# Performance work log

Hardware: AMD Instinct MI355X
Metric: run time of the kernel (lower is better)

The kernel has to match this reference:

```python
import jax, jax.numpy as jnp
import numpy as np

N, E, D, H, Z = 100000, 1600000, 128, 256, 64


def _gconv(x, src, dst, W, b, n):
    # DGL GraphConv, norm='both': D_in^{-1/2} A D_out^{-1/2} x W + b
    ones = jnp.ones(src.shape, x.dtype)
    deg_out = jnp.clip(jax.ops.segment_sum(ones, src, num_segments=n), 1.0)
    deg_in = jnp.clip(jax.ops.segment_sum(ones, dst, num_segments=n), 1.0)
    h = x * (deg_out ** -0.5)[:, None]          # scale by src out-degree
    agg = jax.ops.segment_sum(h[src], dst, num_segments=n)  # SpMM gather/scatter
    return (agg * (deg_in ** -0.5)[:, None]) @ W + b


def setup_inputs() -> dict:
    key = jax.random.key(0)
    ks = jax.random.split(key, 8)
    return {
        "features": jax.random.normal(ks[0], (N, D), jnp.float32),
        "src": jax.random.randint(ks[1], (E,), 0, N, jnp.int32),
        "dst": jax.random.randint(ks[2], (E,), 0, N, jnp.int32),
        "eps": jax.random.normal(ks[3], (N, Z), jnp.float32),
        "W1": jax.random.normal(ks[4], (D, H), jnp.float32) * (1.0 / np.sqrt(D)),
        "b1": jnp.zeros((H,), jnp.float32),
        "W2": jax.random.normal(ks[5], (H, 2 * Z), jnp.float32) * (1.0 / np.sqrt(H)),
        "b2": jnp.zeros((2 * Z,), jnp.float32),
        "W3": jax.random.normal(ks[6], (Z, D), jnp.float32) * (1.0 / np.sqrt(Z)),
        "b3": jnp.zeros((D,), jnp.float32),
    }


def reference(features, src, dst, eps, W1, b1, W2, b2, W3, b3):
    n = features.shape[0]
    h = jax.nn.relu(_gconv(features, src, dst, W1, b1, n))
    mean_logvar = _gconv(h, src, dst, W2, b2, n)
    mean, log_var = jnp.split(mean_logvar, 2, axis=1)
    z = eps * jnp.exp(0.5 * log_var) + mean  # reparameterization
    recon = _gconv(z, src, dst, W3, b3, n)
    return recon, mean, log_var
```

## Files before the change

kernel.cpp:

```cpp
#include <hip/hip_runtime.h>
#include <math.h>


#define MAXD 64

typedef short short8 __attribute__((ext_vector_type(8)));
typedef float f32x4 __attribute__((ext_vector_type(4)));

__device__ __forceinline__ unsigned short f2bf(float f) {
  union { float f; unsigned u; } c; c.f = f;
  unsigned r = c.u + 0x7FFF + ((c.u >> 16) & 1);
  return (unsigned short)(r >> 16);
}
__device__ __forceinline__ float bf2f(unsigned short b) {
  return __builtin_bit_cast(float, (unsigned)b << 16);
}

__global__ __launch_bounds__(256) void k_hist4(const int* __restrict__ src,
    const int* __restrict__ dst, int* __restrict__ degout, int* __restrict__ cnt,
    int* __restrict__ ebuf, int E) {
  int t = blockIdx.x * 256 + threadIdx.x;
  int e0 = t * 4;
  if (e0 + 4 <= E) {
    int4 s4 = *(const int4*)(src + e0);
    int4 d4 = *(const int4*)(dst + e0);
    atomicAdd(&degout[s4.x], 1);
    atomicAdd(&degout[s4.y], 1);
    atomicAdd(&degout[s4.z], 1);
    atomicAdd(&degout[s4.w], 1);
    int p0 = atomicAdd(&cnt[d4.x], 1);
    int p1 = atomicAdd(&cnt[d4.y], 1);
    int p2 = atomicAdd(&cnt[d4.z], 1);
    int p3 = atomicAdd(&cnt[d4.w], 1);
    if (p0 < MAXD) __builtin_nontemporal_store(s4.x, &ebuf[d4.x * MAXD + p0]);
    if (p1 < MAXD) __builtin_nontemporal_store(s4.y, &ebuf[d4.y * MAXD + p1]);
    if (p2 < MAXD) __builtin_nontemporal_store(s4.z, &ebuf[d4.z * MAXD + p2]);
    if (p3 < MAXD) __builtin_nontemporal_store(s4.w, &ebuf[d4.w * MAXD + p3]);
  } else {
    for (int e = e0; e < E; e++) {
      int s = src[e], d = dst[e];
      atomicAdd(&degout[s], 1);
      int p = atomicAdd(&cnt[d], 1);
      if (p < MAXD) __builtin_nontemporal_store(s, &ebuf[d * MAXD + p]);
    }
  }
}

__global__ __launch_bounds__(256) void k_scale(const int* __restrict__ degout,
    const int* __restrict__ cnt, float* __restrict__ sout,
    float* __restrict__ sin_, int N) {
  int i = blockIdx.x * 256 + threadIdx.x;
  if (i >= N) return;
  int dO = degout[i]; if (dO < 1) dO = 1;
  int dI = cnt[i];    if (dI < 1) dI = 1;
  sout[i] = rsqrtf((float)dO);
  sin_[i] = rsqrtf((float)dI);
}

__global__ __launch_bounds__(256) void k_cvt(const float* __restrict__ in,
    unsigned short* __restrict__ out, int n) {
  int i = (blockIdx.x * 256 + threadIdx.x) * 4;
  if (i >= n) return;
  float4 f = *(const float4*)(in + i);
  unsigned lo = (unsigned)f2bf(f.x) | ((unsigned)f2bf(f.y) << 16);
  unsigned hi = (unsigned)f2bf(f.z) | ((unsigned)f2bf(f.w) << 16);
  uint2 o; o.x = lo; o.y = hi;
  *(uint2*)(out + i) = o;
}

template <int K, int OC>
__global__ __launch_bounds__(256) void k_wrepack(const float* __restrict__ W,
    short* __restrict__ Wp) {
  constexpr int KC = K / 32;
  constexpr int TOT = (OC / 16) * KC * 64;
  int t = blockIdx.x * 256 + threadIdx.x;
  if (t >= TOT) return;
  int lane = t & 63;
  int kc = (t >> 6) % KC;
  int nt = t / (KC * 64);
  int n = nt * 16 + (lane & 15);
  int k0 = kc * 32 + ((lane >> 4) * 8);
  short8 v;
  #pragma unroll
  for (int j = 0; j < 8; j++) v[j] = (short)f2bf(W[(size_t)(k0 + j) * OC + n]);
  *(short8*)(Wp + (size_t)t * 8) = v;
}

template <int K, int OC, bool RELU, bool BIAS, bool OUTBF16>
__global__ __launch_bounds__(256) void k_gemm_mfma(
    const unsigned short* __restrict__ A, const short* __restrict__ Wp,
    const float* __restrict__ bias, void* __restrict__ Cout, int N) {
  constexpr int KC = K / 32;
  constexpr int NT = OC / 16;
  int lane = threadIdx.x & 63;
  int wv = threadIdx.x >> 6;
  int m0 = (blockIdx.x * 4 + wv) * 16;
  if (m0 >= N) return;
  int mrow = m0 + (lane & 15);
  if (mrow >= N) mrow = N - 1;
  int q = lane >> 4;
  short8 av[KC];
  #pragma unroll
  for (int kc = 0; kc < KC; kc++)
    av[kc] = *(const short8*)(A + (size_t)mrow * K + kc * 32 + q * 8);
  int col0 = lane & 15;
  int rbase = m0 + q * 4;
  #pragma unroll
  for (int nt = 0; nt < NT; nt++) {
    f32x4 acc = {0.f, 0.f, 0.f, 0.f};
    #pragma unroll
    for (int kc = 0; kc < KC; kc++) {
      short8 bv = *(const short8*)(Wp + ((size_t)(nt * KC + kc) * 64 + lane) * 8);
      acc = __builtin_amdgcn_mfma_f32_16x16x32_bf16(av[kc], bv, acc, 0, 0, 0);
    }
    int col = nt * 16 + col0;
    float bb = BIAS ? bias[col] : 0.f;
    #pragma unroll
    for (int r = 0; r < 4; r++) {
      int row = rbase + r;
      if (row < N) {
        float v = acc[r] + bb;
        if (RELU) v = fmaxf(v, 0.f);
        if (OUTBF16) ((unsigned short*)Cout)[(size_t)row * OC + col] = f2bf(v);
        else         ((float*)Cout)[(size_t)row * OC + col] = v;
      }
    }
  }
}

__global__ __launch_bounds__(256) void k_spmm128b(const unsigned short* __restrict__ x,
    const int* __restrict__ ebuf, const int* __restrict__ cnt,
    const float* __restrict__ sout, const float* __restrict__ sin_,
    unsigned short* __restrict__ out, int N) {
  int lane = threadIdx.x & 63;
  int v = blockIdx.x * 4 + (threadIdx.x >> 6);
  if (v >= N) return;
  v = __builtin_amdgcn_readfirstlane(v);
  int c = cnt[v]; c = c < MAXD ? c : MAXD;
  const int* el = ebuf + (size_t)v * MAXD;
  int u_l = 0; float w_l = 0.f;
  if (lane < c) { u_l = el[lane]; w_l = sout[u_l]; }
  float ax = 0.f, ay = 0.f;
  int i = 0;
  for (; i + 4 <= c; i += 4) {
    #pragma unroll
    for (int j = 0; j < 4; j++) {
      int u = __shfl(u_l, i + j);
      float w = __shfl(w_l, i + j);
      unsigned p = *(const unsigned*)(x + (size_t)u * 128 + lane * 2);
      float lo = __builtin_bit_cast(float, p << 16);
      float hi = __builtin_bit_cast(float, p & 0xFFFF0000u);
      ax = fmaf(w, lo, ax); ay = fmaf(w, hi, ay);
    }
  }
  for (; i < c; i++) {
    int u = __shfl(u_l, i);
    float w = __shfl(w_l, i);
    unsigned p = *(const unsigned*)(x + (size_t)u * 128 + lane * 2);
    float lo = __builtin_bit_cast(float, p << 16);
    float hi = __builtin_bit_cast(float, p & 0xFFFF0000u);
    ax = fmaf(w, lo, ax); ay = fmaf(w, hi, ay);
  }
  float sv = sin_[v];
  unsigned o = (unsigned)f2bf(sv * ax) | ((unsigned)f2bf(sv * ay) << 16);
  *(unsigned*)(out + (size_t)v * 128 + lane * 2) = o;
}

__global__ __launch_bounds__(256) void k_spmm2b(const unsigned short* __restrict__ hw,
    const int* __restrict__ ebuf, const int* __restrict__ cnt,
    const float* __restrict__ sout, const float* __restrict__ sin_,
    const float* __restrict__ b2, const float* __restrict__ eps,
    float* __restrict__ mean_out, float* __restrict__ logvar_out,
    unsigned short* __restrict__ z, int N) {
  int lane = threadIdx.x & 63;
  int v = blockIdx.x * 4 + (threadIdx.x >> 6);
  if (v >= N) return;
  v = __builtin_amdgcn_readfirstlane(v);
  int c = cnt[v]; c = c < MAXD ? c : MAXD;
  const int* el = ebuf + (size_t)v * MAXD;
  int u_l = 0; float w_l = 0.f;
  if (lane < c) { u_l = el[lane]; w_l = sout[u_l]; }
  float ax = 0.f, ay = 0.f;
  int i = 0;
  for (; i + 4 <= c; i += 4) {
    #pragma unroll
    for (int j = 0; j < 4; j++) {
      int u = __shfl(u_l, i + j);
      float w = __shfl(w_l, i + j);
      unsigned p = *(const unsigned*)(hw + (size_t)u * 128 + lane * 2);
      float lo = __builtin_bit_cast(float, p << 16);
      float hi = __builtin_bit_cast(float, p & 0xFFFF0000u);
      ax = fmaf(w, lo, ax); ay = fmaf(w, hi, ay);
    }
  }
  for (; i < c; i++) {
    int u = __shfl(u_l, i);
    float w = __shfl(w_l, i);
    unsigned p = *(const unsigned*)(hw + (size_t)u * 128 + lane * 2);
    float lo = __builtin_bit_cast(float, p << 16);
    float hi = __builtin_bit_cast(float, p & 0xFFFF0000u);
    ax = fmaf(w, lo, ax); ay = fmaf(w, hi, ay);
  }
  float sv = sin_[v];
  float2 bb = ((const float2*)b2)[lane];
  float mx = fmaf(sv, ax, bb.x);
  float my = fmaf(sv, ay, bb.y);
  if (lane < 32) ((float2*)mean_out)[(size_t)v * 32 + lane] = make_float2(mx, my);
  else           ((float2*)logvar_out)[(size_t)v * 32 + (lane - 32)] = make_float2(mx, my);
  float lx = __shfl(mx, (lane & 31) + 32);
  float ly = __shfl(my, (lane & 31) + 32);
  if (lane < 32) {
    float2 e2 = ((const float2*)eps)[(size_t)v * 32 + lane];
    float zx = fmaf(e2.x, expf(0.5f * lx), mx);
    float zy = fmaf(e2.y, expf(0.5f * ly), my);
    unsigned o = (unsigned)f2bf(zx) | ((unsigned)f2bf(zy) << 16);
    *(unsigned*)(z + (size_t)v * 64 + lane * 2) = o;
  }
}

__global__ __launch_bounds__(256) void k_spmm64b(const unsigned short* __restrict__ z,
    const int* __restrict__ ebuf, const int* __restrict__ cnt,
    const float* __restrict__ sout, const float* __restrict__ sin_,
    unsigned short* __restrict__ aggz, int N) {
  int lane = threadIdx.x & 63;
  int v = blockIdx.x * 4 + (threadIdx.x >> 6);
  if (v >= N) return;
  v = __builtin_amdgcn_readfirstlane(v);
  int c = cnt[v]; c = c < MAXD ? c : MAXD;
  const int* el = ebuf + (size_t)v * MAXD;
  int u_l = 0; float w_l = 0.f;
  if (lane < c) { u_l = el[lane]; w_l = sout[u_l]; }
  float a = 0.f;
  int i = 0;
  for (; i + 8 <= c; i += 8) {
    #pragma unroll
    for (int j = 0; j < 8; j++) {
      int u = __shfl(u_l, i + j);
      float w = __shfl(w_l, i + j);
      a = fmaf(w, bf2f(z[(size_t)u * 64 + lane]), a);
    }
  }
  for (; i < c; i++) {
    int u = __shfl(u_l, i);
    float w = __shfl(w_l, i);
    a = fmaf(w, bf2f(z[(size_t)u * 64 + lane]), a);
  }
  aggz[(size_t)v * 64 + lane] = f2bf(sin_[v] * a);
}

extern "C" void kernel_launch(void* const* d_in, const int* in_sizes, int n_in,
                              void* d_out, int out_size, void* d_ws, size_t ws_size,
                              hipStream_t stream) {
  const float* features = (const float*)d_in[0];
  const int*   src      = (const int*)d_in[1];
  const int*   dst      = (const int*)d_in[2];
  const float* eps      = (const float*)d_in[3];
  const float* W1       = (const float*)d_in[4];
  const float* b1       = (const float*)d_in[5];
  const float* W2       = (const float*)d_in[6];
  const float* b2       = (const float*)d_in[7];
  const float* W3       = (const float*)d_in[8];
  const float* b3       = (const float*)d_in[9];
  const int E = in_sizes[1];
  const int N = in_sizes[3] / 64;
  float* out = (float*)d_out;

  char* ws = (char*)d_ws;
  int* degout = (int*)ws;            ws += (size_t)N * 4;
  int* cnt    = (int*)ws;            ws += (size_t)N * 4;
  int* ebuf   = (int*)ws;            ws += (size_t)N * MAXD * 4;
  float* sout = (float*)ws;          ws += (size_t)N * 4;
  float* sin_ = (float*)ws;          ws += (size_t)N * 4;
  short* W1p  = (short*)ws;          ws += 128 * 256 * 2;
  short* W2p  = (short*)ws;          ws += 256 * 128 * 2;
  short* W3p  = (short*)ws;          ws += 64 * 128 * 2;
  char* R1    = ws;                  ws += (size_t)N * 256;
  char* R2    = ws;                  ws += (size_t)N * 256;

  unsigned short* xb    = (unsigned short*)R1;
  unsigned short* hwb   = (unsigned short*)R1;
  unsigned short* aggzb = (unsigned short*)R1;
  unsigned short* agg1b = (unsigned short*)R2;
  unsigned short* zb    = (unsigned short*)R2;

  unsigned short* h     = (unsigned short*)out;
  float* recon          = out;
  float* mean_out       = out + (size_t)N * 128;
  float* logvar_out     = out + (size_t)N * 192;

  hipMemsetAsync(degout, 0, (size_t)N * 8, stream);

  k_hist4<<<((E + 3) / 4 + 255) / 256, 256, 0, stream>>>(src, dst, degout, cnt, ebuf, E);
  k_scale<<<(N + 255) / 256, 256, 0, stream>>>(degout, cnt, sout, sin_, N);
  k_cvt<<<((N * 128 / 4) + 255) / 256, 256, 0, stream>>>(features, xb, N * 128);
  k_wrepack<128, 256><<<16, 256, 0, stream>>>(W1, W1p);
  k_wrepack<256, 128><<<16, 256, 0, stream>>>(W2, W2p);
  k_wrepack<64, 128><<<4, 256, 0, stream>>>(W3, W3p);

  k_spmm128b<<<(N + 3) / 4, 256, 0, stream>>>(xb, ebuf, cnt, sout, sin_, agg1b, N);
  k_gemm_mfma<128, 256, true, true, true>
      <<<(N + 63) / 64, 256, 0, stream>>>(agg1b, W1p, b1, h, N);

  k_gemm_mfma<256, 128, false, false, true>
      <<<(N + 63) / 64, 256, 0, stream>>>(h, W2p, nullptr, hwb, N);
  k_spmm2b<<<(N + 3) / 4, 256, 0, stream>>>(hwb, ebuf, cnt, sout, sin_, b2, eps,
                                            mean_out, logvar_out, zb, N);

  k_spmm64b<<<(N + 3) / 4, 256, 0, stream>>>(zb, ebuf, cnt, sout, sin_, aggzb, N);
  k_gemm_mfma<64, 128, false, true, false>
      <<<(N + 63) / 64, 256, 0, stream>>>(aggzb, W3p, b3, recon, N);
}
```

Before: 589.0 us.

## Slice histogram atomics by node range and sort per-node edge lists

The edge-histogram kernel now runs 8 times as many blocks. Each block handles only the source and destination nodes whose index bits 11-13 match its slice, so each pass's atomics and edge-list writes hit a smaller, more cache-resident address range. A new kernel then bitonic-sorts each node's neighbor list within a wavefront, so later SpMM gathers visit source rows in ascending order for better locality. The cost is reading src/dst eight times and an extra sort pass over the edge buffer. Nontemporal stores were also replaced by normal stores.

```diff
diff --git a/kernel.cpp b/kernel.cpp
--- a/kernel.cpp
+++ b/kernel.cpp
@@ -3,6 +3,7 @@
 
 
 #define MAXD 64
+#define SL(n) (((n) >> 11) & 7)
 
 typedef short short8 __attribute__((ext_vector_type(8)));
 typedef float f32x4 __attribute__((ext_vector_type(4)));
@@ -16,34 +17,53 @@
   return __builtin_bit_cast(float, (unsigned)b << 16);
 }
 
-__global__ __launch_bounds__(256) void k_hist4(const int* __restrict__ src,
+__global__ __launch_bounds__(256) void k_hist_sl(const int* __restrict__ src,
     const int* __restrict__ dst, int* __restrict__ degout, int* __restrict__ cnt,
     int* __restrict__ ebuf, int E) {
-  int t = blockIdx.x * 256 + threadIdx.x;
+  int sl = blockIdx.x & 7;
+  int t = (blockIdx.x >> 3) * 256 + threadIdx.x;
   int e0 = t * 4;
   if (e0 + 4 <= E) {
     int4 s4 = *(const int4*)(src + e0);
     int4 d4 = *(const int4*)(dst + e0);
-    atomicAdd(&degout[s4.x], 1);
-    atomicAdd(&degout[s4.y], 1);
-    atomicAdd(&degout[s4.z], 1);
-    atomicAdd(&degout[s4.w], 1);
-    int p0 = atomicAdd(&cnt[d4.x], 1);
-    int p1 = atomicAdd(&cnt[d4.y], 1);
-    int p2 = atomicAdd(&cnt[d4.z], 1);
-    int p3 = atomicAdd(&cnt[d4.w], 1);
-    if (p0 < MAXD) __builtin_nontemporal_store(s4.x, &ebuf[d4.x * MAXD + p0]);
-    if (p1 < MAXD) __builtin_nontemporal_store(s4.y, &ebuf[d4.y * MAXD + p1]);
-    if (p2 < MAXD) __builtin_nontemporal_store(s4.z, &ebuf[d4.z * MAXD + p2]);
-    if (p3 < MAXD) __builtin_nontemporal_store(s4.w, &ebuf[d4.w * MAXD + p3]);
+    if (SL(s4.x) == sl) atomicAdd(&degout[s4.x], 1);
+    if (SL(s4.y) == sl) atomicAdd(&degout[s4.y], 1);
+    if (SL(s4.z) == sl) atomicAdd(&degout[s4.z], 1);
+    if (SL(s4.w) == sl) atomicAdd(&degout[s4.w], 1);
+    if (SL(d4.x) == sl) { int p = atomicAdd(&cnt[d4.x], 1); if (p < MAXD) ebuf[d4.x * MAXD + p] = s4.x; }
+    if (SL(d4.y) == sl) { int p = atomicAdd(&cnt[d4.y], 1); if (p < MAXD) ebuf[d4.y * MAXD + p] = s4.y; }
+    if (SL(d4.z) == sl) { int p = atomicAdd(&cnt[d4.z], 1); if (p < MAXD) ebuf[d4.z * MAXD + p] = s4.z; }
+    if (SL(d4.w) == sl) { int p = atomicAdd(&cnt[d4.w], 1); if (p < MAXD) ebuf[d4.w * MAXD + p] = s4.w; }
   } else {
     for (int e = e0; e < E; e++) {
       int s = src[e], d = dst[e];
-      atomicAdd(&degout[s], 1);
-      int p = atomicAdd(&cnt[d], 1);
-      if (p < MAXD) __builtin_nontemporal_store(s, &ebuf[d * MAXD + p]);
-    }
-  }
+      if (SL(s) == sl) atomicAdd(&degout[s], 1);
+      if (SL(d) == sl) { int p = atomicAdd(&cnt[d], 1); if (p < MAXD) ebuf[d * MAXD + p] = s; }
+    }
+  }
+}
+
+__global__ __launch_bounds__(256) void k_sortel(int* __restrict__ ebuf,
+    const int* __restrict__ cnt, int N) {
+  int lane = threadIdx.x & 63;
+  int v = blockIdx.x * 4 + (threadIdx.x >> 6);
+  if (v >= N) return;
+  v = __builtin_amdgcn_readfirstlane(v);
+  int c = cnt[v]; c = c < MAXD ? c : MAXD;
+  int* el = ebuf + (size_t)v * MAXD;
+  int val = (lane < c) ? el[lane] : 0x7FFFFFFF;
+  #pragma unroll
+  for (int k = 2; k <= 64; k <<= 1) {
+    #pragma unroll
+    for (int j = k >> 1; j >= 1; j >>= 1) {
+      int other = __shfl_xor(val, j);
+      bool lower = (lane & j) == 0;
+      bool asc = (lane & k) == 0;
+      int mn = min(val, other), mx = max(val, other);
+      val = (lower == asc) ? mn : mx;
+    }
+  }
+  if (lane < c) el[lane] = val;
 }
 
 __global__ __launch_bounds__(256) void k_scale(const int* __restrict__ degout,
@@ -290,7 +310,9 @@
 
   hipMemsetAsync(degout, 0, (size_t)N * 8, stream);
 
-  k_hist4<<<((E + 3) / 4 + 255) / 256, 256, 0, stream>>>(src, dst, degout, cnt, ebuf, E);
+  int bps = ((E + 3) / 4 + 255) / 256;
+  k_hist_sl<<<bps * 8, 256, 0, stream>>>(src, dst, degout, cnt, ebuf, E);
+  k_sortel<<<(N + 3) / 4, 256, 0, stream>>>(ebuf, cnt, N);
   k_scale<<<(N + 255) / 256, 256, 0, stream>>>(degout, cnt, sout, sin_, N);
   k_cvt<<<((N * 128 / 4) + 255) / 256, 256, 0, stream>>>(features, xb, N * 128);
   k_wrepack<128, 256><<<16, 256, 0, stream>>>(W1, W1p);
```

Measured after the change: 589.6 us. About the same (+0.1%).
